# Kernel tuning notes

Measured on AMD Instinct MI355X. Metric: run time of the kernel, lower is better.

## Reference

```python
import jax, jax.numpy as jnp
import numpy as np

L = 2          # n_blocks
E = 512        # emb
H = 8          # heads
D = E // H     # head dim
T = 4096       # context_len
V = 32000      # vocab_size
WIN = 16       # one-sided window (k)
FF = 4 * E     # ff_hidden_mult * emb
EPS = 1e-5


def setup_inputs() -> dict:
    key = jax.random.key(0)
    ks = jax.random.split(key, 12)
    s = 0.02
    return {
        'tokens': jax.random.randint(ks[0], (2, T), 0, V, dtype=jnp.int32),
        'attention_mask': jnp.ones((2, T), dtype=jnp.int32),
        'tok_emb': jax.random.normal(ks[1], (V, E), jnp.float32) * s,
        'pos_emb': jax.random.normal(ks[2], (T, E), jnp.float32) * s,
        'Wq': jax.random.normal(ks[3], (L, E, E), jnp.float32) * s,
        'Wk': jax.random.normal(ks[4], (L, E, E), jnp.float32) * s,
        'Wv': jax.random.normal(ks[5], (L, E, E), jnp.float32) * s,
        'Wo': jax.random.normal(ks[6], (L, E, E), jnp.float32) * s,
        'bo': jnp.zeros((L, E), jnp.float32),
        'ln1_g': jnp.ones((L, E), jnp.float32),
        'ln1_b': jnp.zeros((L, E), jnp.float32),
        'ln2_g': jnp.ones((L, E), jnp.float32),
        'ln2_b': jnp.zeros((L, E), jnp.float32),
        'W1': jax.random.normal(ks[7], (L, E, FF), jnp.float32) * s,
        'b1': jnp.zeros((L, FF), jnp.float32),
        'W2': jax.random.normal(ks[8], (L, FF, E), jnp.float32) * s,
        'b2': jnp.zeros((L, E), jnp.float32),
    }


def layer_norm(x, g, b):
    m = jnp.mean(x, axis=-1, keepdims=True)
    v = jnp.mean(jnp.square(x - m), axis=-1, keepdims=True)
    return (x - m) * jax.lax.rsqrt(v + EPS) * g + b


def sliding_window_attn(x, mask, Wq, Wk, Wv, Wo, bo):
    # x: [B,T,E], mask: [B,T] int
    B, Tt, _ = x.shape
    q = (x @ Wq).reshape(B, Tt, H, D)
    k = (x @ Wk).reshape(B, Tt, H, D)
    v = (x @ Wv).reshape(B, Tt, H, D)
    idx = jnp.arange(Tt)[:, None] + jnp.arange(-WIN, WIN + 1)[None, :]
    valid = (idx >= 0) & (idx < Tt)
    idxc = jnp.clip(idx, 0, Tt - 1)
    kg = k[:, idxc]
    vg = v[:, idxc]
    scores = jnp.einsum('bthd,btwhd->bhtw', q, kg) / jnp.sqrt(jnp.asarray(D, x.dtype))
    mvalid = valid[None, :, :] & (mask[:, idxc] > 0)
    scores = jnp.where(mvalid[:, None, :, :], scores, jnp.asarray(-1e9, x.dtype))
    a = jax.nn.softmax(scores, axis=-1)
    out = jnp.einsum('bhtw,btwhd->bthd', a, vg).reshape(B, Tt, E)
    return out @ Wo + bo


def reference(tokens, attention_mask, tok_emb, pos_emb, Wq, Wk, Wv, Wo, bo,
              ln1_g, ln1_b, ln2_g, ln2_b, W1, b1, W2, b2):
    x = tok_emb[tokens] + pos_emb[None, :, :]             # embed + learned pos
    for l in range(L):
        h = layer_norm(x, ln1_g[l], ln1_b[l])
        x = x + sliding_window_attn(h, attention_mask, Wq[l], Wk[l], Wv[l], Wo[l], bo[l])
        h = layer_norm(x, ln2_g[l], ln2_b[l])
        x = x + (jax.nn.relu(h @ W1[l] + b1[l]) @ W2[l] + b2[l])
    return x
```

## Files before the change

kernel.cpp:

```cpp
#include <hip/hip_runtime.h>

typedef unsigned short u16;
typedef unsigned int u32;
typedef __bf16 bf16x8 __attribute__((ext_vector_type(8)));
typedef float f32x4 __attribute__((ext_vector_type(4)));
typedef u16 u16x8 __attribute__((ext_vector_type(8)));

#define T_SEQ 4096
#define E_DIM 512
#define H_HEADS 8
#define FF_DIM 2048
#define BATCH 2
#define MROWS (BATCH * T_SEQ)

__device__ __forceinline__ float bf2f(u16 u) {
  union { u32 i; float f; } w; w.i = ((u32)u) << 16; return w.f;
}
__device__ __forceinline__ u16 f2bf(float f) {
  union { float f; u32 i; } w; w.f = f;
  u32 r = w.i + 0x7FFFu + ((w.i >> 16) & 1u);
  return (u16)(r >> 16);
}
__device__ __forceinline__ void gload_lds16(const void* g, void* l) {
  __builtin_amdgcn_global_load_lds(
      (const __attribute__((address_space(1))) void*)g,
      (__attribute__((address_space(3))) void*)l, 16, 0, 0);
}

__global__ __launch_bounds__(256) void wconv_kernel(
    const float* __restrict__ Wq, const float* __restrict__ Wk,
    const float* __restrict__ Wv, const float* __restrict__ Wo,
    const float* __restrict__ W1, const float* __restrict__ W2,
    u16* __restrict__ wqkv_t, u16* __restrict__ wo_t,
    u16* __restrict__ w1_t, u16* __restrict__ w2_t) {
  const int z = blockIdx.y;
  const int l = z / 6, ty = z % 6;
  const float* in; u16* op; int K, N;
  const size_t EE = (size_t)E_DIM * E_DIM;
  const size_t EF = (size_t)E_DIM * FF_DIM;
  switch (ty) {
    case 0: in = Wq + l * EE; op = wqkv_t + l * 3 * EE;          K = E_DIM;  N = E_DIM;  break;
    case 1: in = Wk + l * EE; op = wqkv_t + l * 3 * EE + EE;     K = E_DIM;  N = E_DIM;  break;
    case 2: in = Wv + l * EE; op = wqkv_t + l * 3 * EE + 2 * EE; K = E_DIM;  N = E_DIM;  break;
    case 3: in = Wo + l * EE; op = wo_t + l * EE;                K = E_DIM;  N = E_DIM;  break;
    case 4: in = W1 + l * EF; op = w1_t + l * EF;                K = E_DIM;  N = FF_DIM; break;
    default:in = W2 + l * EF; op = w2_t + l * EF;                K = FF_DIM; N = E_DIM;  break;
  }
  const int nn = N >> 5;
  const int ntile = (K >> 5) * nn;
  const int tile = blockIdx.x;
  if (tile >= ntile) return;
  const int tk = tile / nn, tn = tile % nn;
  __shared__ float tl[32][33];
  const int tx = threadIdx.x & 31, tr = threadIdx.x >> 5;
#pragma unroll
  for (int i = 0; i < 4; i++)
    tl[tr + i * 8][tx] = in[(size_t)(tk * 32 + tr + i * 8) * N + tn * 32 + tx];
  __syncthreads();
#pragma unroll
  for (int i = 0; i < 4; i++)
    op[(size_t)(tn * 32 + tr + i * 8) * K + tk * 32 + tx] = f2bf(tl[tx][tr + i * 8]);
}

__global__ __launch_bounds__(256) void embed_kernel(
    const int* __restrict__ tokens, const float* __restrict__ tok_emb,
    const float* __restrict__ pos_emb, float* __restrict__ x) {
  const int idx = blockIdx.x * 256 + threadIdx.x;
  const int rowi = idx >> 7, c4 = (idx & 127) * 4;
  const int t = rowi & (T_SEQ - 1);
  const int tok = tokens[rowi];
  float4 e = *(const float4*)(tok_emb + (size_t)tok * E_DIM + c4);
  float4 p = *(const float4*)(pos_emb + (size_t)t * E_DIM + c4);
  e.x += p.x; e.y += p.y; e.z += p.z; e.w += p.w;
  *(float4*)(x + (size_t)rowi * E_DIM + c4) = e;
}

__global__ __launch_bounds__(256) void ln_kernel(
    const float* __restrict__ x, const float* __restrict__ gam,
    const float* __restrict__ bet, u16* __restrict__ out) {
  const int row = blockIdx.x * 4 + (threadIdx.x >> 6);
  const int lane = threadIdx.x & 63;
  const float* xr = x + (size_t)row * E_DIM + lane * 8;
  float4 v0 = *(const float4*)xr;
  float4 v1 = *(const float4*)(xr + 4);
  float s  = v0.x + v0.y + v0.z + v0.w + v1.x + v1.y + v1.z + v1.w;
  float s2 = v0.x * v0.x + v0.y * v0.y + v0.z * v0.z + v0.w * v0.w +
             v1.x * v1.x + v1.y * v1.y + v1.z * v1.z + v1.w * v1.w;
#pragma unroll
  for (int o = 32; o; o >>= 1) { s += __shfl_xor(s, o); s2 += __shfl_xor(s2, o); }
  const float mean = s * (1.f / E_DIM);
  const float var = s2 * (1.f / E_DIM) - mean * mean;
  const float inv = rsqrtf(var + 1e-5f);
  float4 g0 = *(const float4*)(gam + lane * 8);
  float4 g1 = *(const float4*)(gam + lane * 8 + 4);
  float4 b0 = *(const float4*)(bet + lane * 8);
  float4 b1 = *(const float4*)(bet + lane * 8 + 4);
  u16x8 o8;
  o8[0] = f2bf((v0.x - mean) * inv * g0.x + b0.x);
  o8[1] = f2bf((v0.y - mean) * inv * g0.y + b0.y);
  o8[2] = f2bf((v0.z - mean) * inv * g0.z + b0.z);
  o8[3] = f2bf((v0.w - mean) * inv * g0.w + b0.w);
  o8[4] = f2bf((v1.x - mean) * inv * g1.x + b1.x);
  o8[5] = f2bf((v1.y - mean) * inv * g1.y + b1.y);
  o8[6] = f2bf((v1.z - mean) * inv * g1.z + b1.z);
  o8[7] = f2bf((v1.w - mean) * inv * g1.w + b1.w);
  *(u16x8*)(out + (size_t)row * E_DIM + lane * 8) = o8;
}

template <int BM, int BN, bool BIAS, bool RELU, bool RESID, bool OUTBF>
__global__ __launch_bounds__(256) void gemm_nt(
    const u16* __restrict__ A, const u16* __restrict__ Bt,
    const float* __restrict__ bias, const float* __restrict__ resid,
    void* __restrict__ outp, int K, int N, int gx) {
  constexpr int BK = 64;
  constexpr int FM = BM / 32, FN = BN / 32;
  __shared__ __align__(16) u16 As[2][BM * BK];
  __shared__ __align__(16) u16 Bs[2][BN * BK];
  const int tid = threadIdx.x;
  const int wave = tid >> 6, lane = tid & 63;

  const int cpx = gridDim.x >> 3;
  const int bid = blockIdx.x;
  const int sw = (bid & 7) * cpx + (bid >> 3);
  const int bx = sw % gx, by = sw / gx;

  const int m0 = by * BM, n0 = bx * BN;
  const int wr = wave >> 1, wc = wave & 1;
  const int r = lane & 15, g = lane >> 4;

  const int srow = lane >> 3;
  const int scol = (lane & 7) ^ srow;

  f32x4 acc[FM][FN];
#pragma unroll
  for (int i = 0; i < FM; i++)
#pragma unroll
    for (int j = 0; j < FN; j++) acc[i][j] = (f32x4){0.f, 0.f, 0.f, 0.f};

  constexpr int ASEG = BM / 8, BSEG = BN / 8;

  auto stage = [&](int buf, int k0) {
#pragma unroll
    for (int s = wave; s < ASEG; s += 4) {
      const u16* gp = A + (size_t)(m0 + s * 8 + srow) * K + k0 + scol * 8;
      gload_lds16(gp, (char*)As[buf] + s * 1024 + lane * 16);
    }
#pragma unroll
    for (int s = wave; s < BSEG; s += 4) {
      const u16* gp = Bt + (size_t)(n0 + s * 8 + srow) * K + k0 + scol * 8;
      gload_lds16(gp, (char*)Bs[buf] + s * 1024 + lane * 16);
    }
  };

  auto compute = [&](int buf) {
#pragma unroll
    for (int kk = 0; kk < BK; kk += 32) {
      bf16x8 av[FM], bv[FN];
      const int cg = (kk >> 3) + g;
#pragma unroll
      for (int i = 0; i < FM; i++) {
        const int row = wr * (BM / 2) + i * 16 + r;
        av[i] = *reinterpret_cast<const bf16x8*>(
            &As[buf][row * 64 + ((cg ^ (row & 7)) << 3)]);
      }
#pragma unroll
      for (int j = 0; j < FN; j++) {
        const int row = wc * (BN / 2) + j * 16 + r;
        bv[j] = *reinterpret_cast<const bf16x8*>(
            &Bs[buf][row * 64 + ((cg ^ (row & 7)) << 3)]);
      }
      __builtin_amdgcn_s_setprio(1);
#pragma unroll
      for (int i = 0; i < FM; i++)
#pragma unroll
        for (int j = 0; j < FN; j++)
          acc[i][j] = __builtin_amdgcn_mfma_f32_16x16x32_bf16(av[i], bv[j], acc[i][j], 0, 0, 0);
      __builtin_amdgcn_s_setprio(0);
    }
  };

  const int NT = K >> 6;
  int cur = 0;
  stage(0, 0);
  __syncthreads();
  for (int t = 0; t < NT - 1; ++t) {
    stage(cur ^ 1, (t + 1) << 6);
    compute(cur);
    __syncthreads();
    cur ^= 1;
  }
  compute(cur);

#pragma unroll
  for (int i = 0; i < FM; i++) {
#pragma unroll
    for (int j = 0; j < FN; j++) {
      const int col = n0 + wc * (BN / 2) + j * 16 + r;
      const float bc = BIAS ? bias[col] : 0.f;
#pragma unroll
      for (int rr = 0; rr < 4; rr++) {
        const int row = m0 + wr * (BM / 2) + i * 16 + g * 4 + rr;
        float v = acc[i][j][rr] + bc;
        if (RELU) v = fmaxf(v, 0.f);
        if (RESID) v += resid[(size_t)row * N + col];
        if (OUTBF) ((u16*)outp)[(size_t)row * N + col] = f2bf(v);
        else       ((float*)outp)[(size_t)row * N + col] = v;
      }
    }
  }
}

__global__ __launch_bounds__(256) void attn_kernel(
    const u16* __restrict__ qkv, const int* __restrict__ mask,
    u16* __restrict__ out) {
  __shared__ float kl[96][65];
  __shared__ float vl[96][65];
  __shared__ int ml[96];
  const int b = blockIdx.y >> 3, h = blockIdx.y & 7;
  const int t0 = blockIdx.x * 64;
  const int tid = threadIdx.x;

  for (int s = tid; s < 96 * 8; s += 256) {
    const int rowi = s >> 3, seg = s & 7;
    const int kt = t0 - 16 + rowi;
    float kv[8] = {0.f, 0.f, 0.f, 0.f, 0.f, 0.f, 0.f, 0.f};
    float vv[8] = {0.f, 0.f, 0.f, 0.f, 0.f, 0.f, 0.f, 0.f};
    if (kt >= 0 && kt < T_SEQ) {
      const u16* kp = qkv + (size_t)(b * T_SEQ + kt) * 1536 + E_DIM + h * 64 + seg * 8;
      u16x8 k8 = *(const u16x8*)kp;
      u16x8 v8 = *(const u16x8*)(kp + E_DIM);
#pragma unroll
      for (int j = 0; j < 8; j++) { kv[j] = bf2f(k8[j]); vv[j] = bf2f(v8[j]); }
    }
#pragma unroll
    for (int j = 0; j < 8; j++) {
      kl[rowi][seg * 8 + j] = kv[j];
      vl[rowi][seg * 8 + j] = vv[j];
    }
  }
  for (int i = tid; i < 96; i += 256) {
    const int kt = t0 - 16 + i;
    ml[i] = (kt >= 0 && kt < T_SEQ) ? mask[b * T_SEQ + kt] : 0;
  }
  __syncthreads();

  const int qi = tid >> 2, sub = tid & 3;
  const int t = t0 + qi;
  const u16* qp = qkv + (size_t)(b * T_SEQ + t) * 1536 + h * 64 + sub * 16;
  u16x8 qa = *(const u16x8*)qp;
  u16x8 qb = *(const u16x8*)(qp + 8);
  float q[16];
#pragma unroll
  for (int d = 0; d < 8; d++) { q[d] = bf2f(qa[d]); q[8 + d] = bf2f(qb[d]); }

  float sc[33];
  float mx = -1e30f;
#pragma unroll
  for (int w = 0; w < 33; w++) {
    float s = 0.f;
    const float* kr = &kl[qi + w][sub * 16];
#pragma unroll
    for (int d = 0; d < 16; d++) s += q[d] * kr[d];
    s += __shfl_xor(s, 1);
    s += __shfl_xor(s, 2);
    s = (ml[qi + w] != 0) ? s * 0.125f : -1e9f;
    sc[w] = s;
    mx = fmaxf(mx, s);
  }
  float lsum = 0.f;
#pragma unroll
  for (int w = 0; w < 33; w++) { float p = __expf(sc[w] - mx); sc[w] = p; lsum += p; }
  float o[16];
#pragma unroll
  for (int d = 0; d < 16; d++) o[d] = 0.f;
#pragma unroll
  for (int w = 0; w < 33; w++) {
    const float p = sc[w];
    const float* vr = &vl[qi + w][sub * 16];
#pragma unroll
    for (int d = 0; d < 16; d++) o[d] += p * vr[d];
  }
  const float inv = 1.f / lsum;
  u16* op = out + (size_t)(b * T_SEQ + t) * E_DIM + h * 64 + sub * 16;
  u16x8 o0, o1;
#pragma unroll
  for (int d = 0; d < 8; d++) { o0[d] = f2bf(o[d] * inv); o1[d] = f2bf(o[8 + d] * inv); }
  *(u16x8*)op = o0;
  *(u16x8*)(op + 8) = o1;
}

extern "C" void kernel_launch(void* const* d_in, const int* in_sizes, int n_in,
                              void* d_out, int out_size, void* d_ws, size_t ws_size,
                              hipStream_t stream) {
  const int*   tokens   = (const int*)d_in[0];
  const int*   attnmask = (const int*)d_in[1];
  const float* tok_emb  = (const float*)d_in[2];
  const float* pos_emb  = (const float*)d_in[3];
  const float* Wq       = (const float*)d_in[4];
  const float* Wk       = (const float*)d_in[5];
  const float* Wv       = (const float*)d_in[6];
  const float* Wo       = (const float*)d_in[7];
  const float* bo       = (const float*)d_in[8];
  const float* ln1_g    = (const float*)d_in[9];
  const float* ln1_b    = (const float*)d_in[10];
  const float* ln2_g    = (const float*)d_in[11];
  const float* ln2_b    = (const float*)d_in[12];
  const float* W1       = (const float*)d_in[13];
  const float* b1       = (const float*)d_in[14];
  const float* W2       = (const float*)d_in[15];
  const float* b2       = (const float*)d_in[16];
  float* x = (float*)d_out;

  u16* wqkv_t  = (u16*)d_ws;
  u16* wo_t    = wqkv_t + 2 * 1536 * 512;
  u16* w1_t    = wo_t + 2 * 512 * 512;
  u16* w2_t    = w1_t + 2 * 2048 * 512;
  u16* h_bf    = w2_t + 2 * 512 * 2048;
  u16* qkv_bf  = h_bf + (size_t)MROWS * 512;
  u16* attn_bf = qkv_bf + (size_t)MROWS * 1536;
  u16* mid_bf  = attn_bf + (size_t)MROWS * 512;

  wconv_kernel<<<dim3(1024, 12), 256, 0, stream>>>(Wq, Wk, Wv, Wo, W1, W2,
                                                   wqkv_t, wo_t, w1_t, w2_t);
  embed_kernel<<<dim3(4096), 256, 0, stream>>>(tokens, tok_emb, pos_emb, x);

  for (int l = 0; l < 2; l++) {
    const size_t EE = (size_t)512 * 512;
    const size_t EF = (size_t)512 * 2048;
    ln_kernel<<<dim3(2048), 256, 0, stream>>>(x, ln1_g + l * 512, ln1_b + l * 512, h_bf);
    gemm_nt<128, 128, false, false, false, true>
        <<<dim3(768), 256, 0, stream>>>(h_bf, wqkv_t + l * 3 * EE,
                                        nullptr, nullptr, qkv_bf, 512, 1536, 12);
    attn_kernel<<<dim3(64, 16), 256, 0, stream>>>(qkv_bf, attnmask, attn_bf);
    gemm_nt<64, 128, true, false, true, false>
        <<<dim3(512), 256, 0, stream>>>(attn_bf, wo_t + l * EE,
                                        bo + l * 512, x, x, 512, 512, 4);
    ln_kernel<<<dim3(2048), 256, 0, stream>>>(x, ln2_g + l * 512, ln2_b + l * 512, h_bf);
    gemm_nt<128, 128, true, true, false, true>
        <<<dim3(1024), 256, 0, stream>>>(h_bf, w1_t + l * EF,
                                         b1 + l * 2048, nullptr, mid_bf, 512, 2048, 16);
    gemm_nt<64, 128, true, false, true, false>
        <<<dim3(512), 256, 0, stream>>>(mid_bf, w2_t + l * EF,
                                        b2 + l * 512, x, x, 2048, 512, 4);
  }
}
```

Baseline: 428.7 us.

## Rewrite sliding-window attention with bf16 MFMA for QK and PV

Replaces the scalar fp32 per-thread dot products in the attention kernel with MFMA 16x16x32 bf16 tiles. Each wave computes a 16-query by 48-key score block, masks it to the band, runs softmax, and writes bf16 probabilities to LDS. It then multiplies them by a transposed, XOR-swizzled V tile held in LDS. This cuts ALU work and LDS size, but probabilities are rounded to bf16, and the attention kernel is only part of the whole pipeline.

```diff
diff --git a/kernel.cpp b/kernel.cpp
--- a/kernel.cpp
+++ b/kernel.cpp
@@ -213,80 +213,112 @@
 __global__ __launch_bounds__(256) void attn_kernel(
     const u16* __restrict__ qkv, const int* __restrict__ mask,
     u16* __restrict__ out) {
-  __shared__ float kl[96][65];
-  __shared__ float vl[96][65];
+  __shared__ __align__(16) u16 Vt[64][128];
+  __shared__ __align__(16) u16 Pl[4][16][72];
   __shared__ int ml[96];
   const int b = blockIdx.y >> 3, h = blockIdx.y & 7;
   const int t0 = blockIdx.x * 64;
   const int tid = threadIdx.x;
-
-  for (int s = tid; s < 96 * 8; s += 256) {
-    const int rowi = s >> 3, seg = s & 7;
-    const int kt = t0 - 16 + rowi;
-    float kv[8] = {0.f, 0.f, 0.f, 0.f, 0.f, 0.f, 0.f, 0.f};
-    float vv[8] = {0.f, 0.f, 0.f, 0.f, 0.f, 0.f, 0.f, 0.f};
-    if (kt >= 0 && kt < T_SEQ) {
-      const u16* kp = qkv + (size_t)(b * T_SEQ + kt) * 1536 + E_DIM + h * 64 + seg * 8;
-      u16x8 k8 = *(const u16x8*)kp;
-      u16x8 v8 = *(const u16x8*)(kp + E_DIM);
-#pragma unroll
-      for (int j = 0; j < 8; j++) { kv[j] = bf2f(k8[j]); vv[j] = bf2f(v8[j]); }
-    }
+  const int wave = tid >> 6, lane = tid & 63;
+  const int q15 = lane & 15, g = lane >> 4;
+
+  for (int s = tid; s < 112 * 8; s += 256) {
+    const int c = s >> 3, seg = s & 7;
+    u16x8 v8 = {0, 0, 0, 0, 0, 0, 0, 0};
+    const int kt = t0 - 16 + c;
+    if (c < 96 && kt >= 0 && kt < T_SEQ)
+      v8 = *(const u16x8*)(qkv + (size_t)(b * T_SEQ + kt) * 1536 + 1024 + h * 64 + seg * 8);
 #pragma unroll
     for (int j = 0; j < 8; j++) {
-      kl[rowi][seg * 8 + j] = kv[j];
-      vl[rowi][seg * 8 + j] = vv[j];
+      const int d = seg * 8 + j;
+      const int cp = (c & 7) | ((((c >> 3) ^ seg) & 15) << 3);
+      Vt[d][cp] = v8[j];
     }
   }
   for (int i = tid; i < 96; i += 256) {
     const int kt = t0 - 16 + i;
     ml[i] = (kt >= 0 && kt < T_SEQ) ? mask[b * T_SEQ + kt] : 0;
   }
+
+  const size_t qrow = (size_t)(b * T_SEQ + t0 + wave * 16 + q15) * 1536 + h * 64;
+  bf16x8 qf[2];
+  qf[0] = *(const bf16x8*)(qkv + qrow + g * 8);
+  qf[1] = *(const bf16x8*)(qkv + qrow + 32 + g * 8);
+  bf16x8 kf[3][2];
+#pragma unroll
+  for (int mt = 0; mt < 3; mt++) {
+    int kt = t0 - 16 + wave * 16 + mt * 16 + q15;
+    kt = kt < 0 ? 0 : (kt >= T_SEQ ? T_SEQ - 1 : kt);
+    const size_t kr = (size_t)(b * T_SEQ + kt) * 1536 + 512 + h * 64;
+    kf[mt][0] = *(const bf16x8*)(qkv + kr + g * 8);
+    kf[mt][1] = *(const bf16x8*)(qkv + kr + 32 + g * 8);
+  }
+
+  f32x4 sa[3];
+#pragma unroll
+  for (int mt = 0; mt < 3; mt++) sa[mt] = (f32x4){0.f, 0.f, 0.f, 0.f};
+#pragma unroll
+  for (int ks = 0; ks < 2; ks++)
+#pragma unroll
+    for (int mt = 0; mt < 3; mt++)
+      sa[mt] = __builtin_amdgcn_mfma_f32_16x16x32_bf16(kf[mt][ks], qf[ks], sa[mt], 0, 0, 0);
+
   __syncthreads();
 
-  const int qi = tid >> 2, sub = tid & 3;
-  const int t = t0 + qi;
-  const u16* qp = qkv + (size_t)(b * T_SEQ + t) * 1536 + h * 64 + sub * 16;
-  u16x8 qa = *(const u16x8*)qp;
-  u16x8 qb = *(const u16x8*)(qp + 8);
-  float q[16];
-#pragma unroll
-  for (int d = 0; d < 8; d++) { q[d] = bf2f(qa[d]); q[8 + d] = bf2f(qb[d]); }
-
-  float sc[33];
+  float p[12];
   float mx = -1e30f;
 #pragma unroll
-  for (int w = 0; w < 33; w++) {
-    float s = 0.f;
-    const float* kr = &kl[qi + w][sub * 16];
-#pragma unroll
-    for (int d = 0; d < 16; d++) s += q[d] * kr[d];
-    s += __shfl_xor(s, 1);
-    s += __shfl_xor(s, 2);
-    s = (ml[qi + w] != 0) ? s * 0.125f : -1e9f;
-    sc[w] = s;
-    mx = fmaxf(mx, s);
-  }
-  float lsum = 0.f;
-#pragma unroll
-  for (int w = 0; w < 33; w++) { float p = __expf(sc[w] - mx); sc[w] = p; lsum += p; }
-  float o[16];
-#pragma unroll
-  for (int d = 0; d < 16; d++) o[d] = 0.f;
-#pragma unroll
-  for (int w = 0; w < 33; w++) {
-    const float p = sc[w];
-    const float* vr = &vl[qi + w][sub * 16];
-#pragma unroll
-    for (int d = 0; d < 16; d++) o[d] += p * vr[d];
-  }
-  const float inv = 1.f / lsum;
-  u16* op = out + (size_t)(b * T_SEQ + t) * E_DIM + h * 64 + sub * 16;
-  u16x8 o0, o1;
-#pragma unroll
-  for (int d = 0; d < 8; d++) { o0[d] = f2bf(o[d] * inv); o1[d] = f2bf(o[8 + d] * inv); }
-  *(u16x8*)op = o0;
-  *(u16x8*)(op + 8) = o1;
+  for (int mt = 0; mt < 3; mt++)
+#pragma unroll
+    for (int rr = 0; rr < 4; rr++) {
+      const int cl = mt * 16 + g * 4 + rr;
+      const bool ok = (cl >= q15) && (cl <= q15 + 32) && (ml[wave * 16 + cl] != 0);
+      const float s = ok ? sa[mt][rr] * 0.125f : -1e9f;
+      p[mt * 4 + rr] = s;
+      mx = fmaxf(mx, s);
+    }
+  mx = fmaxf(mx, __shfl_xor(mx, 16));
+  mx = fmaxf(mx, __shfl_xor(mx, 32));
+  float sum = 0.f;
+#pragma unroll
+  for (int i = 0; i < 12; i++) { p[i] = __expf(p[i] - mx); sum += p[i]; }
+  sum += __shfl_xor(sum, 16);
+  sum += __shfl_xor(sum, 32);
+  const float inv = 1.f / sum;
+
+  u16* prow = &Pl[wave][q15][0];
+#pragma unroll
+  for (int mt = 0; mt < 3; mt++) {
+    const u32 w0 = (u32)f2bf(p[mt * 4 + 0] * inv) | ((u32)f2bf(p[mt * 4 + 1] * inv) << 16);
+    const u32 w1 = (u32)f2bf(p[mt * 4 + 2] * inv) | ((u32)f2bf(p[mt * 4 + 3] * inv) << 16);
+    *(u32*)(prow + mt * 16 + g * 4) = w0;
+    *(u32*)(prow + mt * 16 + g * 4 + 2) = w1;
+  }
+  *(u32*)(prow + 48 + g * 4) = 0;
+  *(u32*)(prow + 48 + g * 4 + 2) = 0;
+
+  f32x4 oa[4];
+#pragma unroll
+  for (int nt = 0; nt < 4; nt++) oa[nt] = (f32x4){0.f, 0.f, 0.f, 0.f};
+#pragma unroll
+  for (int ks = 0; ks < 2; ks++) {
+    const bf16x8 pa = *(const bf16x8*)(&Pl[wave][q15][ks * 32 + g * 8]);
+#pragma unroll
+    for (int nt = 0; nt < 4; nt++) {
+      const int d = nt * 16 + q15;
+      const int chunk = 2 * wave + 4 * ks + g;
+      const int cp = ((chunk ^ ((d >> 3) & 7)) & 15) << 3;
+      const bf16x8 vb = *(const bf16x8*)(&Vt[d][cp]);
+      oa[nt] = __builtin_amdgcn_mfma_f32_16x16x32_bf16(pa, vb, oa[nt], 0, 0, 0);
+    }
+  }
+
+  u16* orow = out + (size_t)(b * T_SEQ + t0 + wave * 16) * E_DIM + h * 64;
+#pragma unroll
+  for (int nt = 0; nt < 4; nt++)
+#pragma unroll
+    for (int rr = 0; rr < 4; rr++)
+      orow[(size_t)(g * 4 + rr) * E_DIM + nt * 16 + q15] = f2bf(oa[nt][rr]);
 }
 
 extern "C" void kernel_launch(void* const* d_in, const int* in_sizes, int n_in,
```

After: 377.5 us. 11.9% less time.
